# Kernel tuning notes

Hardware: AMD Instinct MI355X
Metric: run time of the kernel (lower is better)

## Reference

```python
import jax, jax.numpy as jnp
import numpy as np

BATCH, NVIS, NHID, NCOND = 4096, 1024, 4096, 512


def setup_inputs() -> dict:
    key = jax.random.key(0)
    ks = jax.random.split(key, 6)
    return {
        "visible_data": jax.random.uniform(ks[0], (BATCH, NVIS), dtype=jnp.float32),
        "cond_data": jax.random.normal(ks[1], (BATCH, NCOND), dtype=jnp.float32),
        # uniform noise replaces torch.bernoulli's internal RNG: sample = (noise < p)
        "noise": jax.random.uniform(ks[2], (BATCH, NHID), dtype=jnp.float32),
        "W": jax.random.normal(ks[3], (NVIS, NHID), dtype=jnp.float32) * 0.1,
        "b": jnp.zeros((1, NVIS), dtype=jnp.float32),
        "c": jnp.zeros((1, NHID), dtype=jnp.float32),
        "A": jax.random.normal(ks[4], (NCOND, NVIS), dtype=jnp.float32) * 0.1,
        "B": jax.random.normal(ks[5], (NCOND, NHID), dtype=jnp.float32) * 0.1,
    }


def reference(visible_data, cond_data, noise, W, b, c, A, B):
    # sample_h_given_vu: sigmoid(v@W + u@B + c), bernoulli sample via uniform noise
    h1_mean = jax.nn.sigmoid(visible_data @ W + cond_data @ B + c)  # [B, nhid]
    h1_sample = (noise < h1_mean).astype(h1_mean.dtype)
    # sample_v_given_hu (binary): L1-normalized exp == softmax, then argmax one-hot
    pre = h1_sample @ W.T + cond_data @ A + b  # [B, nvis]
    v1_mean = jax.nn.softmax(pre, axis=1)
    max_idx = jnp.argmax(v1_mean, axis=1)
    v1_sample = jax.nn.one_hot(max_idx, pre.shape[1], dtype=pre.dtype)
    return v1_sample
```

## Files before the change

### kernel.cpp

```cpp
#include <hip/hip_runtime.h>
#include <math.h>

static constexpr int BATCH = 4096;
static constexpr int NVIS  = 1024;
static constexpr int NHID  = 4096;
static constexpr int NCOND = 512;

typedef __attribute__((ext_vector_type(8))) short bf16x8;
typedef __attribute__((ext_vector_type(4))) float f32x4;
typedef __attribute__((ext_vector_type(4))) int   i32x4;

static constexpr unsigned HCAP = 131072;
static constexpr unsigned RCAP = 256;
static constexpr size_t MB = 1u << 20;

static constexpr size_t F_WT0   = 0;
static constexpr size_t F_WT1   = F_WT0  + 8*MB;
static constexpr size_t F_BMT0  = F_WT1  + 8*MB;
static constexpr size_t F_BMT1  = F_BMT0 + 4*MB;
static constexpr size_t F_AT0   = F_BMT1 + 4*MB;
static constexpr size_t F_AT1   = F_AT0  + 1*MB;
static constexpr size_t F_V0    = F_AT1  + 1*MB;
static constexpr size_t F_V1    = F_V0   + 8*MB;
static constexpr size_t F_U0    = F_V1   + 8*MB;
static constexpr size_t F_U1    = F_U0   + 4*MB;
static constexpr size_t F_QH    = F_U1   + 4*MB;
static constexpr size_t F_QL    = F_QH   + 4*MB;
static constexpr size_t F_SINV  = F_QL   + 4*MB;
static constexpr size_t F_H     = F_SINV + 8*MB;
static constexpr size_t F_BB    = F_H    + 32*MB;
static constexpr size_t F_HFLAG = F_BB   + 1*MB;
static constexpr size_t F_RFLAG = F_HFLAG + 512*1024;
static constexpr size_t F_RBEST = F_RFLAG + 16384;
static constexpr size_t F_CNT   = F_RBEST + 16384;
static constexpr size_t F_PREB  = F_CNT  + 256;
static constexpr size_t WS_FULL = F_PREB + 2*MB;

__device__ __forceinline__ void gload16(const void* g, void* l) {
    __builtin_amdgcn_global_load_lds(
        (const __attribute__((address_space(1))) void*)g,
        (__attribute__((address_space(3))) void*)l, 16, 0, 0);
}

__device__ __forceinline__ void split1(float x, unsigned short& hi, unsigned short& lo) {
    unsigned u = __float_as_uint(x);
    unsigned r = u + 0x7FFFu + ((u >> 16) & 1u);
    hi = (unsigned short)(r >> 16);
    float rem = x - __uint_as_float(r & 0xFFFF0000u);
    unsigned u2 = __float_as_uint(rem);
    unsigned r2 = u2 + 0x7FFFu + ((u2 >> 16) & 1u);
    lo = (unsigned short)(r2 >> 16);
}

__device__ __forceinline__ void merge3(float& b, unsigned& ix, float& s,
                                       float b2, unsigned i2, float s2) {
    if (b2 > b || (b2 == b && i2 < ix)) { s = fmaxf(b, s2); b = b2; ix = i2; }
    else                                { s = fmaxf(s, b2); }
}

__global__ void kz_zero(unsigned* c) { if (threadIdx.x < 64) c[threadIdx.x] = 0; }

__global__ __launch_bounds__(256) void transpose_split(
    const float* __restrict__ src, int R, int C,
    unsigned short* __restrict__ d0, unsigned short* __restrict__ d1) {
    __shared__ float tile[32][33];
    const int c0 = blockIdx.x * 32, r0 = blockIdx.y * 32;
    const int tx = threadIdx.x & 31, ty = threadIdx.x >> 5;
#pragma unroll
    for (int e = 0; e < 4; ++e)
        tile[ty + e * 8][tx] = src[(size_t)(r0 + ty + e * 8) * C + c0 + tx];
    __syncthreads();
#pragma unroll
    for (int e = 0; e < 4; ++e) {
        int c = c0 + ty + e * 8;
        unsigned short hi, lo;
        split1(tile[tx][ty + e * 8], hi, lo);
        d0[(size_t)c * R + r0 + tx] = hi;
        d1[(size_t)c * R + r0 + tx] = lo;
    }
}

__global__ __launch_bounds__(256) void transpose_f32_all(
    const float* __restrict__ W, const float* __restrict__ Bm, const float* __restrict__ Am,
    float* __restrict__ WTf, float* __restrict__ BmTf, float* __restrict__ ATf) {
    __shared__ float tile[32][33];
    int blk = blockIdx.x;
    const float* src; float* dst; int R, C, bx, by;
    if (blk < 4096)      { src = W;  dst = WTf;  R = 1024; C = 4096; blk -= 0;    bx = blk & 127; by = blk >> 7; }
    else if (blk < 6144) { src = Bm; dst = BmTf; R = 512;  C = 4096; blk -= 4096; bx = blk & 127; by = blk >> 7; }
    else                 { src = Am; dst = ATf;  R = 512;  C = 1024; blk -= 6144; bx = blk & 31;  by = blk >> 5; }
    const int c0 = bx * 32, r0 = by * 32;
    const int tx = threadIdx.x & 31, ty = threadIdx.x >> 5;
#pragma unroll
    for (int e = 0; e < 4; ++e)
        tile[ty + e * 8][tx] = src[(size_t)(r0 + ty + e * 8) * C + c0 + tx];
    __syncthreads();
#pragma unroll
    for (int e = 0; e < 4; ++e)
        dst[(size_t)(c0 + ty + e * 8) * R + r0 + tx] = tile[tx][ty + e * 8];
}

__global__ __launch_bounds__(256) void split_planes(
    const float* __restrict__ src, int n4,
    unsigned short* __restrict__ p0, unsigned short* __restrict__ p1) {
    for (int i = blockIdx.x * 256 + threadIdx.x; i < n4; i += gridDim.x * 256) {
        float4 v = ((const float4*)src)[i];
        unsigned short h0,h1,h2,h3,l0,l1,l2,l3;
        split1(v.x,h0,l0); split1(v.y,h1,l1); split1(v.z,h2,l2); split1(v.w,h3,l3);
        ((ushort4*)p0)[i] = make_ushort4(h0,h1,h2,h3);
        ((ushort4*)p1)[i] = make_ushort4(l0,l1,l2,l3);
    }
}

__global__ __launch_bounds__(256) void quantize_w(
    const float* __restrict__ W, signed char* __restrict__ QH,
    signed char* __restrict__ QL, float* __restrict__ SINV) {
    __shared__ float red[256];
    const int i = blockIdx.x, t = threadIdx.x;
    const float* row = W + (size_t)i * NHID;
    float4 v[4];
    float mx = 0.f;
#pragma unroll
    for (int e = 0; e < 4; ++e) {
        v[e] = *(const float4*)(row + e * 1024 + t * 4);
        mx = fmaxf(mx, fmaxf(fmaxf(fabsf(v[e].x), fabsf(v[e].y)),
                             fmaxf(fabsf(v[e].z), fabsf(v[e].w))));
    }
    red[t] = mx; __syncthreads();
    for (int s = 128; s; s >>= 1) {
        if (t < s) red[t] = fmaxf(red[t], red[t + s]);
        __syncthreads();
    }
    const float rm = fmaxf(red[0], 1e-30f);
    const float sc = 32256.f / rm;
    if (t == 0) SINV[i] = rm / 32256.f;
#pragma unroll
    for (int e = 0; e < 4; ++e) {
        const float* pv = (const float*)&v[e];
        unsigned ph = 0, pl = 0;
#pragma unroll
        for (int j = 0; j < 4; ++j) {
            int wq = (int)lrintf(pv[j] * sc);
            int hi = (wq + 128) >> 8;
            int lo = wq - (hi << 8);
            ph |= ((unsigned)hi & 0xFFu) << (8 * j);
            pl |= ((unsigned)lo & 0xFFu) << (8 * j);
        }
        *(unsigned*)(QH + (size_t)i * NHID + e * 1024 + t * 4) = ph;
        *(unsigned*)(QL + (size_t)i * NHID + e * 1024 + t * 4) = pl;
    }
}

__global__ __launch_bounds__(256, 4) void k1_s4(
    const float* __restrict__ vd, const float* __restrict__ cd,
    const float* __restrict__ noise,
    const unsigned short* __restrict__ WT0, const unsigned short* __restrict__ WT1,
    const unsigned short* __restrict__ BmT0, const unsigned short* __restrict__ BmT1,
    const float* __restrict__ cvec, unsigned char* __restrict__ hout,
    unsigned* __restrict__ hcnt, unsigned* __restrict__ hflag)
{
    __shared__ __align__(16) unsigned short As0[128][32], As1[128][32],
                                            Bs0[128][32], Bs1[128][32];
    const int t = threadIdx.x, lane = t & 63, wid = t >> 6;
    const int g = lane >> 4, cc = lane & 15;
    const int wrow = wid >> 1, wcol = wid & 1;
    const int pc = (g ^ ((cc >> 1) & 3)) * 8;
    const int nwg = gridDim.x * gridDim.y;
    const int bid = blockIdx.y * gridDim.x + blockIdx.x;
    const int q = nwg >> 3;
    const int swz = (bid & 7) * q + (bid >> 3);
    const int b0 = (swz / gridDim.x) * 128;
    const int j0 = (swz % gridDim.x) * 128;

    f32x4 acc[4][4] = {};

    for (int ph = 0; ph < 2; ++ph) {
        const int K = ph ? NCOND : NVIS;
        const float* Asrc = ph ? cd : vd;
        const unsigned short* B0 = ph ? BmT0 : WT0;
        const unsigned short* B1 = ph ? BmT1 : WT1;
        for (int k0 = 0; k0 < K; k0 += 32) {
            __syncthreads();
#pragma unroll
            for (int e = 0; e < 4; ++e) {
                int idx = t + e * 256, row = idx >> 3, qq = idx & 7;
                const float4 v = *(const float4*)(Asrc + (size_t)(b0 + row) * K + k0 + qq * 4);
                unsigned short h0,h1,h2,h3, s0,s1,s2,s3;
                split1(v.x,h0,s0); split1(v.y,h1,s1); split1(v.z,h2,s2); split1(v.w,h3,s3);
                int c = qq >> 1, sc = c ^ ((row >> 1) & 3);
                int pos = sc * 8 + (qq & 1) * 4;
                *(ushort4*)&As0[row][pos] = make_ushort4(h0,h1,h2,h3);
                *(ushort4*)&As1[row][pos] = make_ushort4(s0,s1,s2,s3);
            }
#pragma unroll
            for (int e = 0; e < 2; ++e) {
                int idx = t + e * 256, r = idx >> 2, s = idx & 3;
                int sc = s ^ ((r >> 1) & 3);
                size_t gb = (size_t)(j0 + r) * K + k0 + sc * 8;
                size_t ldd = (size_t)idx * 8;
                gload16(B0 + gb, &Bs0[0][0] + ldd);
                gload16(B1 + gb, &Bs1[0][0] + ldd);
            }
            __syncthreads();
            bf16x8 bb0[4], bb1[4];
#pragma unroll
            for (int ni = 0; ni < 4; ++ni) {
                int n = wcol * 64 + ni * 16 + cc;
                bb0[ni] = *(const bf16x8*)&Bs0[n][pc];
                bb1[ni] = *(const bf16x8*)&Bs1[n][pc];
            }
#pragma unroll
            for (int mi = 0; mi < 4; ++mi) {
                int r = wrow * 64 + mi * 16 + cc;
                bf16x8 a0 = *(const bf16x8*)&As0[r][pc];
                bf16x8 a1 = *(const bf16x8*)&As1[r][pc];
#pragma unroll
                for (int ni = 0; ni < 4; ++ni) {
                    acc[mi][ni] = __builtin_amdgcn_mfma_f32_16x16x32_bf16(a0, bb0[ni], acc[mi][ni], 0, 0, 0);
                    acc[mi][ni] = __builtin_amdgcn_mfma_f32_16x16x32_bf16(a0, bb1[ni], acc[mi][ni], 0, 0, 0);
                    acc[mi][ni] = __builtin_amdgcn_mfma_f32_16x16x32_bf16(a1, bb0[ni], acc[mi][ni], 0, 0, 0);
                }
            }
        }
    }

#pragma unroll
    for (int ni = 0; ni < 4; ++ni) {
        int j = j0 + wcol * 64 + ni * 16 + cc;
        float cj = cvec[j];
#pragma unroll
        for (int mi = 0; mi < 4; ++mi) {
#pragma unroll
            for (int i = 0; i < 4; ++i) {
                int b = b0 + wrow * 64 + mi * 16 + g * 4 + i;
                float z = acc[mi][ni][i] + cj;
                float m = 1.0f / (1.0f + __expf(-z));
                float nv = noise[(size_t)b * NHID + j];
                hout[(size_t)b * NHID + j] = (nv < m) ? (unsigned char)1 : (unsigned char)0;
                if (fabsf(nv - m) < 2.5e-4f) {
                    unsigned p = atomicAdd(hcnt, 1u);
                    if (p < HCAP) hflag[p] = ((unsigned)b << 12) | (unsigned)j;
                }
            }
        }
    }
}

__global__ __launch_bounds__(512, 2) void k2_i8(
    const unsigned char* __restrict__ hbf,
    const unsigned short* __restrict__ U0, const unsigned short* __restrict__ U1,
    const signed char* __restrict__ QH, const signed char* __restrict__ QL,
    const float* __restrict__ SINV,
    const unsigned short* __restrict__ AT0, const unsigned short* __restrict__ AT1,
    const float* __restrict__ bvec, float4* __restrict__ blockbest)
{
    __shared__ __align__(16) char smem[32768];
    __shared__ float4 mbuf[4][128];
    const int t = threadIdx.x, lane = t & 63, wid = t >> 6;
    const int g = lane >> 4, cc = lane & 15;
    const int wrow = wid >> 2, wcol = wid & 3;
    const int pcb = (g ^ ((cc >> 1) & 3)) * 16;
    const int nwg = gridDim.x * gridDim.y;
    const int bid = blockIdx.y * gridDim.x + blockIdx.x;
    const int q = nwg >> 3;
    const int swz = (bid & 7) * q + (bid >> 3);
    const int b0 = (swz / gridDim.x) * 128;
    const int i0 = (swz % gridDim.x) * 128;

    char* Ah  = smem;
    char* Qhs = smem + 8192;
    char* Qls = smem + 16384;

    i32x4 ah[4][2] = {}, al[4][2] = {};

    for (int k0 = 0; k0 < NHID; k0 += 64) {
        __syncthreads();
        {
            int r = t >> 2, s = t & 3, sc = s ^ ((r >> 1) & 3);
            size_t off = (size_t)r * 64 + s * 16;
            gload16(hbf + (size_t)(b0 + r) * NHID + k0 + sc * 16, Ah + off);
            gload16(QH + (size_t)(i0 + r) * NHID + k0 + sc * 16, Qhs + off);
            gload16(QL + (size_t)(i0 + r) * NHID + k0 + sc * 16, Qls + off);
        }
        __syncthreads();
        i32x4 bh[2], bl[2];
#pragma unroll
        for (int ni = 0; ni < 2; ++ni) {
            int n = wcol * 32 + ni * 16 + cc;
            bh[ni] = *(const i32x4*)(Qhs + (size_t)n * 64 + pcb);
            bl[ni] = *(const i32x4*)(Qls + (size_t)n * 64 + pcb);
        }
#pragma unroll
        for (int mi = 0; mi < 4; ++mi) {
            i32x4 a = *(const i32x4*)(Ah + (size_t)(wrow * 64 + mi * 16 + cc) * 64 + pcb);
#pragma unroll
            for (int ni = 0; ni < 2; ++ni) {
                ah[mi][ni] = __builtin_amdgcn_mfma_i32_16x16x64_i8(a, bh[ni], ah[mi][ni], 0, 0, 0);
                al[mi][ni] = __builtin_amdgcn_mfma_i32_16x16x64_i8(a, bl[ni], al[mi][ni], 0, 0, 0);
            }
        }
    }
    f32x4 acc[4][2];
#pragma unroll
    for (int ni = 0; ni < 2; ++ni) {
        int col = i0 + wcol * 32 + ni * 16 + cc;
        float sv = SINV[col];
#pragma unroll
        for (int mi = 0; mi < 4; ++mi)
#pragma unroll
            for (int e = 0; e < 4; ++e)
                acc[mi][ni][e] = fmaf(256.f, (float)ah[mi][ni][e], (float)al[mi][ni][e]) * sv;
    }

    char* As0 = smem;
    char* As1 = smem + 8192;
    char* Bs0 = smem + 16384;
    char* Bs1 = smem + 24576;
    for (int k0 = 0; k0 < NCOND; k0 += 32) {
        __syncthreads();
        {
            int r = t >> 2, s = t & 3, sc = s ^ ((r >> 1) & 3);
            size_t off = (size_t)r * 64 + s * 16;
            size_t ga = (size_t)(b0 + r) * NCOND + k0 + sc * 8;
            gload16(U0 + ga, As0 + off);
            gload16(U1 + ga, As1 + off);
            size_t go = (size_t)(i0 + r) * NCOND + k0 + sc * 8;
            gload16(AT0 + go, Bs0 + off);
            gload16(AT1 + go, Bs1 + off);
        }
        __syncthreads();
        bf16x8 bb0[2], bb1[2];
#pragma unroll
        for (int ni = 0; ni < 2; ++ni) {
            int n = wcol * 32 + ni * 16 + cc;
            bb0[ni] = *(const bf16x8*)(Bs0 + (size_t)n * 64 + pcb);
            bb1[ni] = *(const bf16x8*)(Bs1 + (size_t)n * 64 + pcb);
        }
#pragma unroll
        for (int mi = 0; mi < 4; ++mi) {
            int r = wrow * 64 + mi * 16 + cc;
            bf16x8 a0 = *(const bf16x8*)(As0 + (size_t)r * 64 + pcb);
            bf16x8 a1 = *(const bf16x8*)(As1 + (size_t)r * 64 + pcb);
#pragma unroll
            for (int ni = 0; ni < 2; ++ni) {
                acc[mi][ni] = __builtin_amdgcn_mfma_f32_16x16x32_bf16(a0, bb0[ni], acc[mi][ni], 0, 0, 0);
                acc[mi][ni] = __builtin_amdgcn_mfma_f32_16x16x32_bf16(a0, bb1[ni], acc[mi][ni], 0, 0, 0);
                acc[mi][ni] = __builtin_amdgcn_mfma_f32_16x16x32_bf16(a1, bb0[ni], acc[mi][ni], 0, 0, 0);
            }
        }
    }

#pragma unroll
    for (int ni = 0; ni < 2; ++ni) {
        int colb = i0 + wcol * 32 + ni * 16 + cc;
        float bb = bvec[colb];
#pragma unroll
        for (int mi = 0; mi < 4; ++mi)
#pragma unroll
            for (int i = 0; i < 4; ++i) acc[mi][ni][i] += bb;
    }
#pragma unroll
    for (int mi = 0; mi < 4; ++mi) {
#pragma unroll
        for (int i = 0; i < 4; ++i) {
            float best = acc[mi][0][i];
            unsigned bidx = (unsigned)(i0 + wcol * 32 + cc);
            float sec = -3.4e38f;
            merge3(best, bidx, sec, acc[mi][1][i],
                   (unsigned)(i0 + wcol * 32 + 16 + cc), -3.4e38f);
#pragma unroll
            for (int m = 1; m < 16; m <<= 1) {
                float ob = __shfl_xor(best, m);
                unsigned oi = __shfl_xor(bidx, m);
                float os = __shfl_xor(sec, m);
                merge3(best, bidx, sec, ob, oi, os);
            }
            if (cc == 0)
                mbuf[wcol][wrow * 64 + mi * 16 + g * 4 + i] =
                    make_float4(best, sec, __uint_as_float(bidx), 0.f);
        }
    }
    __syncthreads();
    if (t < 128) {
        float4 f0 = mbuf[0][t];
        float best = f0.x, sec = f0.y;
        unsigned bidx = __float_as_uint(f0.z);
#pragma unroll
        for (int wq = 1; wq < 4; ++wq) {
            float4 fq = mbuf[wq][t];
            merge3(best, bidx, sec, fq.x, __float_as_uint(fq.z), fq.y);
        }
        blockbest[(size_t)(b0 + t) * 8 + (unsigned)(i0 >> 7)] =
            make_float4(best, sec, __uint_as_float(bidx), 0.f);
    }
}

__global__ __launch_bounds__(256) void k5_recheck_h(
    const float* __restrict__ vd, const float* __restrict__ cd, const float* __restrict__ noise,
    const float* __restrict__ WTf, const float* __restrict__ BmTf, const float* __restrict__ cvec,
    const unsigned* __restrict__ hcnt, const unsigned* __restrict__ hflag,
    unsigned char* __restrict__ h) {
    const int gw = (blockIdx.x * 256 + threadIdx.x) >> 6, lane = threadIdx.x & 63;
    const int nw = gridDim.x * 4;
    unsigned n = *hcnt; if (n > HCAP) n = HCAP;
    for (unsigned e = gw; e < n; e += nw) {
        unsigned p = hflag[e];
        int b = p >> 12, j = p & 4095;
        double s = 0.0;
        for (int k = lane; k < NVIS; k += 64)
            s += (double)vd[(size_t)b * NVIS + k] * (double)WTf[(size_t)j * NVIS + k];
        for (int k = lane; k < NCOND; k += 64)
            s += (double)cd[(size_t)b * NCOND + k] * (double)BmTf[(size_t)j * NCOND + k];
        for (int m = 32; m; m >>= 1) s += __shfl_xor(s, m);
        if (lane == 0) {
            double z = s + (double)cvec[j];
            double mm = 1.0 / (1.0 + exp(-z));
            h[(size_t)b * NHID + j] =
                ((double)noise[(size_t)b * NHID + j] < mm) ? (unsigned char)1 : (unsigned char)0;
        }
    }
}

__global__ __launch_bounds__(256) void k3_merge8(
    const float4* __restrict__ blockbest, unsigned* __restrict__ rowbest,
    unsigned* __restrict__ rcnt, unsigned* __restrict__ rowflag) {
    const int t = threadIdx.x;
    const int row = blockIdx.x * 32 + (t >> 3), e = t & 7;
    float4 f = blockbest[(size_t)row * 8 + e];
    float best = f.x, sec = f.y;
    unsigned idx = __float_as_uint(f.z);
#pragma unroll
    for (int m = 1; m < 8; m <<= 1) {
        float ob = __shfl_xor(best, m);
        unsigned oi = __shfl_xor(idx, m);
        float os = __shfl_xor(sec, m);
        merge3(best, idx, sec, ob, oi, os);
    }
    if (e == 0) {
        rowbest[row] = idx;
        if (best - sec < 4e-3f) {
            unsigned p = atomicAdd(rcnt, 1u);
            if (p < 4096) rowflag[p] = (unsigned)row;
        }
    }
}

__global__ __launch_bounds__(256) void k_onehot(const unsigned* __restrict__ rowbest,
                                                float* __restrict__ out) {
    const int row = blockIdx.x;
    const unsigned idx = rowbest[row];
    const int base = threadIdx.x * 4;
    float4 o;
    o.x = (base + 0 == (int)idx) ? 1.f : 0.f;
    o.y = (base + 1 == (int)idx) ? 1.f : 0.f;
    o.z = (base + 2 == (int)idx) ? 1.f : 0.f;
    o.w = (base + 3 == (int)idx) ? 1.f : 0.f;
    *(float4*)(out + (size_t)row * NVIS + base) = o;
}

__global__ __launch_bounds__(256) void k6_rows_pre(
    const unsigned char* __restrict__ h, const float* __restrict__ cd,
    const float* __restrict__ W, const float* __restrict__ ATf, const float* __restrict__ bvec,
    const unsigned* __restrict__ rcnt, const unsigned* __restrict__ rowflag,
    double* __restrict__ prebuf) {
    const int gw = (blockIdx.x * 256 + threadIdx.x) >> 6, lane = threadIdx.x & 63;
    const int nw = gridDim.x * 4;
    unsigned n = *rcnt; if (n > RCAP) n = RCAP;
    for (unsigned e = gw; e < n * 1024u; e += nw) {
        int ri = e >> 10, i = e & 1023;
        int b = (int)rowflag[ri];
        double s = 0.0;
        for (int k = lane; k < NHID; k += 64) {
            double hv = h[(size_t)b * NHID + k] ? 1.0 : 0.0;
            s += hv * (double)W[(size_t)i * NHID + k];
        }
        for (int k = lane; k < NCOND; k += 64)
            s += (double)cd[(size_t)b * NCOND + k] * (double)ATf[(size_t)i * NCOND + k];
        for (int m = 32; m; m >>= 1) s += __shfl_xor(s, m);
        if (lane == 0) prebuf[(size_t)ri * 1024 + i] = s + (double)bvec[i];
    }
}

__global__ __launch_bounds__(256) void k6_rows_argmax(
    const unsigned* __restrict__ rcnt, const unsigned* __restrict__ rowflag,
    const double* __restrict__ prebuf, float* __restrict__ out) {
    __shared__ double sv[256];
    __shared__ int si[256];
    unsigned n = *rcnt; if (n > RCAP) n = RCAP;
    const int t = threadIdx.x;
    for (unsigned ri = blockIdx.x; ri < n; ri += gridDim.x) {
        const int row = (int)rowflag[ri];
        const double* pr = prebuf + (size_t)ri * 1024;
        double best = pr[t * 4];
        int bi = t * 4;
#pragma unroll
        for (int e = 1; e < 4; ++e) {
            double v = pr[t * 4 + e];
            if (v > best) { best = v; bi = t * 4 + e; }
        }
        sv[t] = best; si[t] = bi;
        __syncthreads();
        for (int s = 128; s; s >>= 1) {
            if (t < s) {
                double v2 = sv[t + s]; int i2 = si[t + s];
                if (v2 > sv[t] || (v2 == sv[t] && i2 < si[t])) { sv[t] = v2; si[t] = i2; }
            }
            __syncthreads();
        }
        const int amax = si[0];
        const int base = t * 4;
        float4 o;
        o.x = (base + 0 == amax) ? 1.f : 0.f;
        o.y = (base + 1 == amax) ? 1.f : 0.f;
        o.z = (base + 2 == amax) ? 1.f : 0.f;
        o.w = (base + 3 == amax) ? 1.f : 0.f;
        *(float4*)(out + (size_t)row * NVIS + base) = o;
        __syncthreads();
    }
}

extern "C" void kernel_launch(void* const* d_in, const int* in_sizes, int n_in,
                              void* d_out, int out_size, void* d_ws, size_t ws_size,
                              hipStream_t stream) {
    const float* vd = (const float*)d_in[0];
    const float* cd = (const float*)d_in[1];
    const float* nz = (const float*)d_in[2];
    const float* W  = (const float*)d_in[3];
    const float* bv = (const float*)d_in[4];
    const float* cv = (const float*)d_in[5];
    const float* Am = (const float*)d_in[6];
    const float* Bm = (const float*)d_in[7];
    float* out = (float*)d_out;
    char* w = (char*)d_ws;

    unsigned short* WT0  = (unsigned short*)(w + F_WT0);
    unsigned short* WT1  = (unsigned short*)(w + F_WT1);
    unsigned short* BmT0 = (unsigned short*)(w + F_BMT0);
    unsigned short* BmT1 = (unsigned short*)(w + F_BMT1);
    unsigned short* AT0  = (unsigned short*)(w + F_AT0);
    unsigned short* AT1  = (unsigned short*)(w + F_AT1);
    unsigned short* U0   = (unsigned short*)(w + F_U0);
    unsigned short* U1   = (unsigned short*)(w + F_U1);
    signed char*    QH   = (signed char*)(w + F_QH);
    signed char*    QL   = (signed char*)(w + F_QL);
    float*          SINV = (float*)(w + F_SINV);
    unsigned char*  hbf  = (unsigned char*)(w + F_H);
    float4*   blockbest  = (float4*)(w + F_BB);
    unsigned* hflag      = (unsigned*)(w + F_HFLAG);
    unsigned* rowflag    = (unsigned*)(w + F_RFLAG);
    unsigned* rowbest    = (unsigned*)(w + F_RBEST);
    unsigned* counters   = (unsigned*)(w + F_CNT);
    double*   prebuf     = (double*)(w + F_PREB);
    unsigned* hcnt = &counters[0];
    unsigned* rcnt = &counters[1];
    float* WTf32  = (float*)(w + F_V0);
    float* BmTf32 = (float*)(w + F_WT0);
    float* ATf32  = (float*)(w + F_WT1);

    dim3 blk(256);
    kz_zero<<<1, 64, 0, stream>>>(counters);
    transpose_split<<<dim3(NHID / 32, NVIS / 32), blk, 0, stream>>>(W, NVIS, NHID, WT0, WT1);
    transpose_split<<<dim3(NHID / 32, NCOND / 32), blk, 0, stream>>>(Bm, NCOND, NHID, BmT0, BmT1);
    transpose_split<<<dim3(NVIS / 32, NCOND / 32), blk, 0, stream>>>(Am, NCOND, NVIS, AT0, AT1);
    split_planes<<<2048, blk, 0, stream>>>(cd, BATCH * NCOND / 4, U0, U1);
    quantize_w<<<NVIS, blk, 0, stream>>>(W, QH, QL, SINV);
    k1_s4<<<dim3(NHID / 128, BATCH / 128), blk, 0, stream>>>(
        vd, cd, nz, WT0, WT1, BmT0, BmT1, cv, hbf, hcnt, hflag);
    transpose_f32_all<<<6656, blk, 0, stream>>>(W, Bm, Am, WTf32, BmTf32, ATf32);
    k5_recheck_h<<<256, blk, 0, stream>>>(vd, cd, nz, WTf32, BmTf32, cv, hcnt, hflag, hbf);
    k2_i8<<<dim3(NVIS / 128, BATCH / 128), 512, 0, stream>>>(
        hbf, U0, U1, QH, QL, SINV, AT0, AT1, bv, blockbest);
    k3_merge8<<<BATCH / 32, blk, 0, stream>>>(blockbest, rowbest, rcnt, rowflag);
    k_onehot<<<BATCH, blk, 0, stream>>>(rowbest, out);
    k6_rows_pre<<<512, blk, 0, stream>>>(hbf, cd, W, ATf32, bv, rcnt, rowflag, prebuf);
    k6_rows_argmax<<<64, blk, 0, stream>>>(rcnt, rowflag, prebuf, out);
}
```

Measured before the change: 574.3 us.

## Enlarge hidden GEMM tile to 256x256 and pre-split visible data into bf16 planes

The first GEMM kernel now uses 256x256 output tiles with 512 threads and 8x4 MFMA accumulators per wave, and loads both operands directly into LDS via async 16-byte loads. The visible data is pre-split into hi/lo bf16 planes by an extra split_planes launch, removing the in-kernel fp32-to-bf16 split. This raises operand reuse per LDS load but reduces the grid to 256 blocks and increases register pressure, and adds a pass over the visible matrix.

```diff
diff --git a/kernel.cpp b/kernel.cpp
--- a/kernel.cpp
+++ b/kernel.cpp
@@ -151,75 +151,65 @@
     }
 }
 
-__global__ __launch_bounds__(256, 4) void k1_s4(
-    const float* __restrict__ vd, const float* __restrict__ cd,
+__global__ __launch_bounds__(512, 2) void k1_t2(
     const float* __restrict__ noise,
+    const unsigned short* __restrict__ V0, const unsigned short* __restrict__ V1,
+    const unsigned short* __restrict__ U0, const unsigned short* __restrict__ U1,
     const unsigned short* __restrict__ WT0, const unsigned short* __restrict__ WT1,
     const unsigned short* __restrict__ BmT0, const unsigned short* __restrict__ BmT1,
     const float* __restrict__ cvec, unsigned char* __restrict__ hout,
     unsigned* __restrict__ hcnt, unsigned* __restrict__ hflag)
 {
-    __shared__ __align__(16) unsigned short As0[128][32], As1[128][32],
-                                            Bs0[128][32], Bs1[128][32];
+    __shared__ __align__(16) unsigned short As0[256][32], As1[256][32],
+                                            Bs0[256][32], Bs1[256][32];
     const int t = threadIdx.x, lane = t & 63, wid = t >> 6;
     const int g = lane >> 4, cc = lane & 15;
-    const int wrow = wid >> 1, wcol = wid & 1;
+    const int wrow = wid >> 2, wcol = wid & 3;
     const int pc = (g ^ ((cc >> 1) & 3)) * 8;
     const int nwg = gridDim.x * gridDim.y;
     const int bid = blockIdx.y * gridDim.x + blockIdx.x;
     const int q = nwg >> 3;
     const int swz = (bid & 7) * q + (bid >> 3);
-    const int b0 = (swz / gridDim.x) * 128;
-    const int j0 = (swz % gridDim.x) * 128;
-
-    f32x4 acc[4][4] = {};
-
-    for (int ph = 0; ph < 2; ++ph) {
-        const int K = ph ? NCOND : NVIS;
-        const float* Asrc = ph ? cd : vd;
-        const unsigned short* B0 = ph ? BmT0 : WT0;
-        const unsigned short* B1 = ph ? BmT1 : WT1;
-        for (int k0 = 0; k0 < K; k0 += 32) {
-            __syncthreads();
-#pragma unroll
-            for (int e = 0; e < 4; ++e) {
-                int idx = t + e * 256, row = idx >> 3, qq = idx & 7;
-                const float4 v = *(const float4*)(Asrc + (size_t)(b0 + row) * K + k0 + qq * 4);
-                unsigned short h0,h1,h2,h3, s0,s1,s2,s3;
-                split1(v.x,h0,s0); split1(v.y,h1,s1); split1(v.z,h2,s2); split1(v.w,h3,s3);
-                int c = qq >> 1, sc = c ^ ((row >> 1) & 3);
-                int pos = sc * 8 + (qq & 1) * 4;
-                *(ushort4*)&As0[row][pos] = make_ushort4(h0,h1,h2,h3);
-                *(ushort4*)&As1[row][pos] = make_ushort4(s0,s1,s2,s3);
-            }
-#pragma unroll
-            for (int e = 0; e < 2; ++e) {
-                int idx = t + e * 256, r = idx >> 2, s = idx & 3;
-                int sc = s ^ ((r >> 1) & 3);
-                size_t gb = (size_t)(j0 + r) * K + k0 + sc * 8;
-                size_t ldd = (size_t)idx * 8;
-                gload16(B0 + gb, &Bs0[0][0] + ldd);
-                gload16(B1 + gb, &Bs1[0][0] + ldd);
-            }
-            __syncthreads();
-            bf16x8 bb0[4], bb1[4];
+    const int b0 = (swz / gridDim.x) * 256;
+    const int j0 = (swz % gridDim.x) * 256;
+
+    f32x4 acc[8][4] = {};
+
+    for (int tt = 0; tt < 48; ++tt) {
+        const unsigned short *A0_, *A1_, *B0_, *B1_; int K_, k0_;
+        if (tt < 32) { A0_ = V0; A1_ = V1; B0_ = WT0; B1_ = WT1; K_ = 1024; k0_ = tt * 32; }
+        else         { A0_ = U0; A1_ = U1; B0_ = BmT0; B1_ = BmT1; K_ = 512; k0_ = (tt - 32) * 32; }
+        __syncthreads();
+#pragma unroll
+        for (int e = 0; e < 2; ++e) {
+            int idx = t + e * 512, r = idx >> 2, s = idx & 3;
+            int sc = s ^ ((r >> 1) & 3);
+            size_t ga = (size_t)(b0 + r) * K_ + k0_ + sc * 8;
+            size_t gb = (size_t)(j0 + r) * K_ + k0_ + sc * 8;
+            size_t ldd = (size_t)idx * 8;
+            gload16(A0_ + ga, &As0[0][0] + ldd);
+            gload16(A1_ + ga, &As1[0][0] + ldd);
+            gload16(B0_ + gb, &Bs0[0][0] + ldd);
+            gload16(B1_ + gb, &Bs1[0][0] + ldd);
+        }
+        __syncthreads();
+        bf16x8 bb0[4], bb1[4];
+#pragma unroll
+        for (int ni = 0; ni < 4; ++ni) {
+            int n = wcol * 64 + ni * 16 + cc;
+            bb0[ni] = *(const bf16x8*)&Bs0[n][pc];
+            bb1[ni] = *(const bf16x8*)&Bs1[n][pc];
+        }
+#pragma unroll
+        for (int mi = 0; mi < 8; ++mi) {
+            int r = wrow * 128 + mi * 16 + cc;
+            bf16x8 a0 = *(const bf16x8*)&As0[r][pc];
+            bf16x8 a1 = *(const bf16x8*)&As1[r][pc];
 #pragma unroll
             for (int ni = 0; ni < 4; ++ni) {
-                int n = wcol * 64 + ni * 16 + cc;
-                bb0[ni] = *(const bf16x8*)&Bs0[n][pc];
-                bb1[ni] = *(const bf16x8*)&Bs1[n][pc];
-            }
-#pragma unroll
-            for (int mi = 0; mi < 4; ++mi) {
-                int r = wrow * 64 + mi * 16 + cc;
-                bf16x8 a0 = *(const bf16x8*)&As0[r][pc];
-                bf16x8 a1 = *(const bf16x8*)&As1[r][pc];
-#pragma unroll
-                for (int ni = 0; ni < 4; ++ni) {
-                    acc[mi][ni] = __builtin_amdgcn_mfma_f32_16x16x32_bf16(a0, bb0[ni], acc[mi][ni], 0, 0, 0);
-                    acc[mi][ni] = __builtin_amdgcn_mfma_f32_16x16x32_bf16(a0, bb1[ni], acc[mi][ni], 0, 0, 0);
-                    acc[mi][ni] = __builtin_amdgcn_mfma_f32_16x16x32_bf16(a1, bb0[ni], acc[mi][ni], 0, 0, 0);
-                }
+                acc[mi][ni] = __builtin_amdgcn_mfma_f32_16x16x32_bf16(a0, bb0[ni], acc[mi][ni], 0, 0, 0);
+                acc[mi][ni] = __builtin_amdgcn_mfma_f32_16x16x32_bf16(a0, bb1[ni], acc[mi][ni], 0, 0, 0);
+                acc[mi][ni] = __builtin_amdgcn_mfma_f32_16x16x32_bf16(a1, bb0[ni], acc[mi][ni], 0, 0, 0);
             }
         }
     }
@@ -229,10 +219,10 @@
         int j = j0 + wcol * 64 + ni * 16 + cc;
         float cj = cvec[j];
 #pragma unroll
-        for (int mi = 0; mi < 4; ++mi) {
+        for (int mi = 0; mi < 8; ++mi) {
 #pragma unroll
             for (int i = 0; i < 4; ++i) {
-                int b = b0 + wrow * 64 + mi * 16 + g * 4 + i;
+                int b = b0 + wrow * 128 + mi * 16 + g * 4 + i;
                 float z = acc[mi][ni][i] + cj;
                 float m = 1.0f / (1.0f + __expf(-z));
                 float nv = noise[(size_t)b * NHID + j];
@@ -539,6 +529,8 @@
     unsigned short* BmT1 = (unsigned short*)(w + F_BMT1);
     unsigned short* AT0  = (unsigned short*)(w + F_AT0);
     unsigned short* AT1  = (unsigned short*)(w + F_AT1);
+    unsigned short* V0   = (unsigned short*)(w + F_V0);
+    unsigned short* V1   = (unsigned short*)(w + F_V1);
     unsigned short* U0   = (unsigned short*)(w + F_U0);
     unsigned short* U1   = (unsigned short*)(w + F_U1);
     signed char*    QH   = (signed char*)(w + F_QH);
@@ -562,10 +554,11 @@
     transpose_split<<<dim3(NHID / 32, NVIS / 32), blk, 0, stream>>>(W, NVIS, NHID, WT0, WT1);
     transpose_split<<<dim3(NHID / 32, NCOND / 32), blk, 0, stream>>>(Bm, NCOND, NHID, BmT0, BmT1);
     transpose_split<<<dim3(NVIS / 32, NCOND / 32), blk, 0, stream>>>(Am, NCOND, NVIS, AT0, AT1);
+    split_planes<<<2048, blk, 0, stream>>>(vd, BATCH * NVIS / 4, V0, V1);
     split_planes<<<2048, blk, 0, stream>>>(cd, BATCH * NCOND / 4, U0, U1);
     quantize_w<<<NVIS, blk, 0, stream>>>(W, QH, QL, SINV);
-    k1_s4<<<dim3(NHID / 128, BATCH / 128), blk, 0, stream>>>(
-        vd, cd, nz, WT0, WT1, BmT0, BmT1, cv, hbf, hcnt, hflag);
+    k1_t2<<<dim3(NHID / 256, BATCH / 256), 512, 0, stream>>>(
+        nz, V0, V1, U0, U1, WT0, WT1, BmT0, BmT1, cv, hbf, hcnt, hflag);
     transpose_f32_all<<<6656, blk, 0, stream>>>(W, Bm, Am, WTf32, BmTf32, ATf32);
     k5_recheck_h<<<256, blk, 0, stream>>>(vd, cd, nz, WTf32, BmTf32, cv, hcnt, hflag, hbf);
     k2_i8<<<dim3(NVIS / 128, BATCH / 128), 512, 0, stream>>>(
```

Result: faster. 528.8 us (-7.9%).
